# Kernel optimization log

Hardware: AMD Instinct MI355X
Metric: run time of the kernel (lower is better)

## Reference

```python
import jax, jax.numpy as jnp
import numpy as np

D_MODEL = 1024
H = 16
D_K = D_MODEL // H
B = 4
S = 2048


def setup_inputs() -> dict:
    key = jax.random.key(0)
    kq, kk, kv, k1, k2, k3, k4 = jax.random.split(key, 7)
    scale = 1.0 / np.sqrt(D_MODEL)
    inputs = {
        "query": jax.random.normal(kq, (B, S, D_MODEL), dtype=jnp.float32),
        "key": jax.random.normal(kk, (B, S, D_MODEL), dtype=jnp.float32),
        "value": jax.random.normal(kv, (B, S, D_MODEL), dtype=jnp.float32),
        # causal mask: True = masked (upper triangle above diagonal)
        "mask": jnp.triu(jnp.ones((1, 1, S, S), dtype=bool), k=1),
        # nn.Linear weights stored as (out, in); y = x @ W.T
        "w_q": jax.random.normal(k1, (D_MODEL, D_MODEL), dtype=jnp.float32) * scale,
        "w_k": jax.random.normal(k2, (D_MODEL, D_MODEL), dtype=jnp.float32) * scale,
        "w_v": jax.random.normal(k3, (D_MODEL, D_MODEL), dtype=jnp.float32) * scale,
        "w_o": jax.random.normal(k4, (D_MODEL, D_MODEL), dtype=jnp.float32) * scale,
    }
    return inputs


def reference(query, key, value, mask, w_q, w_k, w_v, w_o):
    batch = query.shape[0]

    def split_heads(x):  # (B, S, D) -> (B, H, S, d_k)
        return x.reshape(batch, -1, H, D_K).transpose(0, 2, 1, 3)

    q = split_heads(query @ w_q.T)
    k = split_heads(key @ w_k.T)
    v = split_heads(value @ w_v.T)

    scores = jnp.einsum("bhqd,bhkd->bhqk", q, k) / jnp.sqrt(jnp.float32(D_K))
    scores = jnp.where(mask, -jnp.inf, scores)
    attn = jax.nn.softmax(scores, axis=-1)
    out = jnp.einsum("bhqk,bhkd->bhqd", attn, v)  # (B, H, Sq, d_v)
    out = out.transpose(0, 2, 1, 3).reshape(batch, -1, D_MODEL)
    return out @ w_o.T
```

## Files before the change

### kernel.cpp

```cpp
#include <hip/hip_runtime.h>

typedef unsigned short u16;
typedef __bf16 bf16x8 __attribute__((ext_vector_type(8)));
typedef float f32x4 __attribute__((ext_vector_type(4)));

__device__ __forceinline__ u16 f2bf(float f) {
  union { float f; unsigned u; } v; v.f = f;
  unsigned r = v.u + 0x7fffu + ((v.u >> 16) & 1u);
  return (u16)(r >> 16);
}

__device__ __forceinline__ u16 f2bfn(float f) {
  union { __bf16 h; u16 u; } v; v.h = (__bf16)f; return v.u;
}

__device__ __forceinline__ void gload_lds16(const void* g, void* l) {
  using gvp = const __attribute__((address_space(1))) void*;
  using lvp = __attribute__((address_space(3))) void*;
  __builtin_amdgcn_global_load_lds((gvp)g, (lvp)l, 16, 0, 0);
}

__global__ void cvt_bf16(const float* __restrict__ s0, const float* __restrict__ s1,
                         const float* __restrict__ s2, const float* __restrict__ s3,
                         u16* __restrict__ d0, u16* __restrict__ d1,
                         u16* __restrict__ d2, u16* __restrict__ d3, int n4) {
  const float* srcs[4] = {s0, s1, s2, s3};
  u16* dsts[4] = {d0, d1, d2, d3};
  const float4* src = (const float4*)srcs[blockIdx.y];
  u16* dst = dsts[blockIdx.y];
  for (int i = blockIdx.x * blockDim.x + threadIdx.x; i < n4; i += gridDim.x * blockDim.x) {
    float4 v = src[i];
    ushort4 o;
    o.x = f2bf(v.x); o.y = f2bf(v.y); o.z = f2bf(v.z); o.w = f2bf(v.w);
    *(ushort4*)(dst + (size_t)i * 4) = o;
  }
}

template<int MODE>
__global__ __launch_bounds__(256)
void gemm_bt(const u16* __restrict__ A, const u16* __restrict__ Bw, void* __restrict__ Cout) {
  constexpr int N = 1024, K = 1024, BK = 64;
  __shared__ u16 As[128 * BK];
  __shared__ u16 Bs[128 * BK];
  const int tid = threadIdx.x;
  const int lane = tid & 63, wave = tid >> 6;
  const int wm = wave >> 1, wn = wave & 1;
  const int l15 = lane & 15, lhi = lane >> 4;
  const int m0 = blockIdx.y * 128, n0 = blockIdx.x * 128;
  const int r0 = tid >> 3;
  const int o8 = (tid & 7) * 8;

  f32x4 acc[4][4] = {};

  for (int kt = 0; kt < K / BK; ++kt) {
    const int kb = kt * BK;
#pragma unroll
    for (int c = 0; c < 4; ++c) {
      const int row = c * 32 + r0;
      gload_lds16(A + (m0 + row) * K + kb + o8, (char*)As + (c * 256 + tid) * 16);
      gload_lds16(Bw + (n0 + row) * K + kb + o8, (char*)Bs + (c * 256 + tid) * 16);
    }
    __syncthreads();
#pragma unroll
    for (int kk = 0; kk < 2; ++kk) {
      bf16x8 a[4], b[4];
#pragma unroll
      for (int i = 0; i < 4; ++i)
        a[i] = *(const bf16x8*)(As + (wm * 64 + i * 16 + l15) * BK + kk * 32 + lhi * 8);
#pragma unroll
      for (int j = 0; j < 4; ++j)
        b[j] = *(const bf16x8*)(Bs + (wn * 64 + j * 16 + l15) * BK + kk * 32 + lhi * 8);
#pragma unroll
      for (int i = 0; i < 4; ++i)
#pragma unroll
        for (int j = 0; j < 4; ++j)
          acc[i][j] = __builtin_amdgcn_mfma_f32_16x16x32_bf16(a[i], b[j], acc[i][j], 0, 0, 0);
    }
    __syncthreads();
  }

#pragma unroll
  for (int i = 0; i < 4; ++i) {
#pragma unroll
    for (int j = 0; j < 4; ++j) {
#pragma unroll
      for (int r = 0; r < 4; ++r) {
        const int mg = m0 + wm * 64 + i * 16 + lhi * 4 + r;
        const int ng = n0 + wn * 64 + j * 16 + l15;
        const float v = acc[i][j][r];
        if (MODE == 0) {
          ((float*)Cout)[(size_t)mg * N + ng] = v;
        } else {
          const int b = mg >> 11, s = mg & 2047, h = ng >> 6, dk = ng & 63;
          if (MODE == 1)
            ((u16*)Cout)[(((size_t)(b * 16 + h) * 2048 + s) << 6) + dk] = f2bf(v);
          else
            ((u16*)Cout)[((size_t)(b * 16 + h) * 64 + dk) * 2048 + s] = f2bf(v);
        }
      }
    }
  }
}

__global__ __launch_bounds__(256)
void attn_fwd(const u16* __restrict__ Q, const u16* __restrict__ Kh,
              const u16* __restrict__ Vt, u16* __restrict__ Ao) {
  constexpr int S = 2048;
  constexpr float SCL = 0.125f * 1.44269504088896f;
  __shared__ u16 Ks[2][64 * 64];
  __shared__ u16 Vs[2][64 * 64];
  __shared__ u16 Ps[4][16 * 64];
  const int tid = threadIdx.x;
  const int lane = tid & 63, w = tid >> 6;
  const int l15 = lane & 15, lhi = lane >> 4;
  const int bh = blockIdx.y;
  const int qtA = 31 - (int)blockIdx.x;
  const int qtB = (int)blockIdx.x;

  const u16* QbA = Q + ((size_t)bh * S + qtA * 64 + w * 16 + l15) * 64;
  const u16* QbB = Q + ((size_t)bh * S + qtB * 64 + w * 16 + l15) * 64;
  const bf16x8 qfA0 = *(const bf16x8*)(QbA + lhi * 8);
  const bf16x8 qfA1 = *(const bf16x8*)(QbA + 32 + lhi * 8);
  const bf16x8 qfB0 = *(const bf16x8*)(QbB + lhi * 8);
  const bf16x8 qfB1 = *(const bf16x8*)(QbB + 32 + lhi * 8);

  f32x4 o_acc[4] = {};
  float mrow[4] = {-1e30f, -1e30f, -1e30f, -1e30f};
  float lrow[4] = {0.f, 0.f, 0.f, 0.f};

  const int r0 = tid >> 3;
  const int o16 = (tid & 7) * 16;
  const int gcb = o16 ^ ((r0 & 7) << 4);
  char* PsB = (char*)(Ps[w]);

  auto STAGE = [&](int b, int kt) {
#pragma unroll
    for (int c = 0; c < 2; ++c) {
      const int row = c * 32 + r0;
      gload_lds16((const char*)Kh + ((size_t)(bh * S + kt * 64 + row) * 64) * 2 + gcb,
                  (char*)(Ks[b]) + (c * 256 + tid) * 16);
      gload_lds16((const char*)Vt + ((size_t)(bh * 64 + row) * S + kt * 64) * 2 + gcb,
                  (char*)(Vs[b]) + (c * 256 + tid) * 16);
    }
  };

  const int bb = bh >> 4, hh = bh & 15;
  auto EPILOGUE = [&](int qt) {
#pragma unroll
    for (int r = 0; r < 4; ++r) {
      const float inv = 1.0f / lrow[r];
      const int sg = qt * 64 + w * 16 + lhi * 4 + r;
#pragma unroll
      for (int c = 0; c < 4; ++c)
        Ao[(((size_t)(bb * 2048 + sg) * 16 + hh) << 6) + c * 16 + l15] = f2bfn(o_acc[c][r] * inv);
    }
  };

  const int stepsA = qtA + 1;
  const int total = stepsA + qtB + 1;

  STAGE(0, 0);
  __syncthreads();
  int buf = 0;

  for (int step = 0; step < total; ++step) {
    const bool phB = step >= stepsA;
    const int qt = phB ? qtB : qtA;
    const int kt = phB ? step - stepsA : step;

    if (step + 1 < total)
      STAGE(buf ^ 1, (step + 1 >= stepsA) ? step + 1 - stepsA : step + 1);

    const char* KsB = (const char*)(Ks[buf]);
    const char* VsB = (const char*)(Vs[buf]);
    const bf16x8 q0 = phB ? qfB0 : qfA0;
    const bf16x8 q1 = phB ? qfB1 : qfA1;

    f32x4 sA[4];
    __builtin_amdgcn_s_setprio(1);
#pragma unroll
    for (int c = 0; c < 4; ++c) {
      f32x4 z = {};
      const int krow = c * 16 + l15;
      const int swz = (krow & 7) << 4;
      z = __builtin_amdgcn_mfma_f32_16x16x32_bf16(
          q0, *(const bf16x8*)(KsB + ((krow * 128 + lhi * 16) ^ swz)), z, 0, 0, 0);
      z = __builtin_amdgcn_mfma_f32_16x16x32_bf16(
          q1, *(const bf16x8*)(KsB + ((krow * 128 + 64 + lhi * 16) ^ swz)), z, 0, 0, 0);
      sA[c] = z;
    }
    __builtin_amdgcn_s_setprio(0);

    const bool diag = (kt == qt);
#pragma unroll
    for (int c = 0; c < 4; ++c)
#pragma unroll
      for (int r = 0; r < 4; ++r) {
        float sv = sA[c][r] * SCL;
        if (diag && (c * 16 + l15 > w * 16 + lhi * 4 + r)) sv = -1e30f;
        sA[c][r] = sv;
      }

#pragma unroll
    for (int r = 0; r < 4; ++r) {
      float tm = fmaxf(fmaxf(sA[0][r], sA[1][r]), fmaxf(sA[2][r], sA[3][r]));
      tm = fmaxf(tm, __shfl_xor(tm, 1));
      tm = fmaxf(tm, __shfl_xor(tm, 2));
      tm = fmaxf(tm, __shfl_xor(tm, 4));
      tm = fmaxf(tm, __shfl_xor(tm, 8));
      const float mnew = fmaxf(mrow[r], tm);
      const float sc = __builtin_amdgcn_exp2f(mrow[r] - mnew);
      float rs = 0.f;
#pragma unroll
      for (int c = 0; c < 4; ++c) {
        const float p = __builtin_amdgcn_exp2f(sA[c][r] - mnew);
        sA[c][r] = p;
        rs += p;
      }
      rs += __shfl_xor(rs, 1);
      rs += __shfl_xor(rs, 2);
      rs += __shfl_xor(rs, 4);
      rs += __shfl_xor(rs, 8);
      lrow[r] = lrow[r] * sc + rs;
      mrow[r] = mnew;
#pragma unroll
      for (int c = 0; c < 4; ++c) o_acc[c][r] *= sc;
    }

#pragma unroll
    for (int c = 0; c < 4; ++c)
#pragma unroll
      for (int r = 0; r < 4; ++r) {
        const int prow = lhi * 4 + r;
        *(u16*)(PsB + ((prow * 128 + (c * 16 + l15) * 2) ^ ((prow & 7) << 4))) = f2bfn(sA[c][r]);
      }

    bf16x8 pa0 = *(const bf16x8*)(PsB + ((l15 * 128 + lhi * 16) ^ ((l15 & 7) << 4)));
    bf16x8 pa1 = *(const bf16x8*)(PsB + ((l15 * 128 + 64 + lhi * 16) ^ ((l15 & 7) << 4)));
    __builtin_amdgcn_s_setprio(1);
#pragma unroll
    for (int c = 0; c < 4; ++c) {
      const int drow = c * 16 + l15;
      const int swz = (drow & 7) << 4;
      o_acc[c] = __builtin_amdgcn_mfma_f32_16x16x32_bf16(
          pa0, *(const bf16x8*)(VsB + ((drow * 128 + lhi * 16) ^ swz)), o_acc[c], 0, 0, 0);
      o_acc[c] = __builtin_amdgcn_mfma_f32_16x16x32_bf16(
          pa1, *(const bf16x8*)(VsB + ((drow * 128 + 64 + lhi * 16) ^ swz)), o_acc[c], 0, 0, 0);
    }
    __builtin_amdgcn_s_setprio(0);

    __syncthreads();
    buf ^= 1;

    if (step == stepsA - 1) {
      EPILOGUE(qtA);
#pragma unroll
      for (int r = 0; r < 4; ++r) { mrow[r] = -1e30f; lrow[r] = 0.f; }
#pragma unroll
      for (int c = 0; c < 4; ++c) o_acc[c] = f32x4{};
    }
  }

  EPILOGUE(qtB);
}

extern "C" void kernel_launch(void* const* d_in, const int* in_sizes, int n_in,
                              void* d_out, int out_size, void* d_ws, size_t ws_size,
                              hipStream_t stream) {
  const float* q  = (const float*)d_in[0];
  const float* k  = (const float*)d_in[1];
  const float* v  = (const float*)d_in[2];
  const float* wq = (const float*)d_in[4];
  const float* wk = (const float*)d_in[5];
  const float* wv = (const float*)d_in[6];
  const float* wo = (const float*)d_in[7];

  char* ws = (char*)d_ws;
  const size_t SZX = (size_t)8192 * 1024 * 2;
  const size_t SZW = (size_t)1024 * 1024 * 2;
  u16* Xq = (u16*)(ws);
  u16* Xk = (u16*)(ws + SZX);
  u16* Xv = (u16*)(ws + 2 * SZX);
  u16* Wq = (u16*)(ws + 3 * SZX);
  u16* Wk = (u16*)(ws + 3 * SZX + SZW);
  u16* Wv = (u16*)(ws + 3 * SZX + 2 * SZW);
  u16* Wo = (u16*)(ws + 3 * SZX + 3 * SZW);
  u16* Qh = (u16*)(ws + 3 * SZX + 4 * SZW);
  u16* Kh = (u16*)(ws + 4 * SZX + 4 * SZW);
  u16* Vt = (u16*)(ws + 5 * SZX + 4 * SZW);
  u16* Ao = Xq;

  cvt_bf16<<<dim3(1024, 3), 256, 0, stream>>>(q, k, v, q, Xq, Xk, Xv, Xq, 8388608 / 4);
  cvt_bf16<<<dim3(256, 4), 256, 0, stream>>>(wq, wk, wv, wo, Wq, Wk, Wv, Wo, 1048576 / 4);
  gemm_bt<1><<<dim3(8, 64), 256, 0, stream>>>(Xq, Wq, Qh);
  gemm_bt<1><<<dim3(8, 64), 256, 0, stream>>>(Xk, Wk, Kh);
  gemm_bt<2><<<dim3(8, 64), 256, 0, stream>>>(Xv, Wv, Vt);
  attn_fwd<<<dim3(16, 64), 256, 0, stream>>>(Qh, Kh, Vt, Ao);
  gemm_bt<0><<<dim3(8, 64), 256, 0, stream>>>(Ao, Wo, (float*)d_out);
}
```

Before: 415.3 us.

## Transpose QK^T MFMA so each lane owns one query row for softmax

Swaps the MFMA operands in the QK^T product so the score tile comes out transposed, with each lane holding a single query row spread across its 16 accumulator values. Row max and sum then need mostly in-register reductions plus two cross-lane shuffles instead of four shuffles per row for four rows. P is written to LDS with packed 8-byte stores instead of scalar 2-byte stores. In exchange, the rescale factors must be shuffled back to the output accumulator layout each step and in the epilogue, and the causal mask indexing changes to match.

```diff
diff --git a/kernel.cpp b/kernel.cpp
--- a/kernel.cpp
+++ b/kernel.cpp
@@ -125,8 +125,7 @@
   const bf16x8 qfB1 = *(const bf16x8*)(QbB + 32 + lhi * 8);
 
   f32x4 o_acc[4] = {};
-  float mrow[4] = {-1e30f, -1e30f, -1e30f, -1e30f};
-  float lrow[4] = {0.f, 0.f, 0.f, 0.f};
+  float mrow = -1e30f, lrow = 0.f;
 
   const int r0 = tid >> 3;
   const int o16 = (tid & 7) * 16;
@@ -148,7 +147,7 @@
   auto EPILOGUE = [&](int qt) {
 #pragma unroll
     for (int r = 0; r < 4; ++r) {
-      const float inv = 1.0f / lrow[r];
+      const float inv = 1.0f / __shfl(lrow, lhi * 4 + r);
       const int sg = qt * 64 + w * 16 + lhi * 4 + r;
 #pragma unroll
       for (int c = 0; c < 4; ++c)
@@ -184,9 +183,9 @@
       const int krow = c * 16 + l15;
       const int swz = (krow & 7) << 4;
       z = __builtin_amdgcn_mfma_f32_16x16x32_bf16(
-          q0, *(const bf16x8*)(KsB + ((krow * 128 + lhi * 16) ^ swz)), z, 0, 0, 0);
+          *(const bf16x8*)(KsB + ((krow * 128 + lhi * 16) ^ swz)), q0, z, 0, 0, 0);
       z = __builtin_amdgcn_mfma_f32_16x16x32_bf16(
-          q1, *(const bf16x8*)(KsB + ((krow * 128 + 64 + lhi * 16) ^ swz)), z, 0, 0, 0);
+          *(const bf16x8*)(KsB + ((krow * 128 + 64 + lhi * 16) ^ swz)), q1, z, 0, 0, 0);
       sA[c] = z;
     }
     __builtin_amdgcn_s_setprio(0);
@@ -197,43 +196,53 @@
 #pragma unroll
       for (int r = 0; r < 4; ++r) {
         float sv = sA[c][r] * SCL;
-        if (diag && (c * 16 + l15 > w * 16 + lhi * 4 + r)) sv = -1e30f;
+        if (diag && (c * 16 + lhi * 4 + r > w * 16 + l15)) sv = -1e30f;
         sA[c][r] = sv;
       }
 
-#pragma unroll
-    for (int r = 0; r < 4; ++r) {
-      float tm = fmaxf(fmaxf(sA[0][r], sA[1][r]), fmaxf(sA[2][r], sA[3][r]));
-      tm = fmaxf(tm, __shfl_xor(tm, 1));
-      tm = fmaxf(tm, __shfl_xor(tm, 2));
-      tm = fmaxf(tm, __shfl_xor(tm, 4));
-      tm = fmaxf(tm, __shfl_xor(tm, 8));
-      const float mnew = fmaxf(mrow[r], tm);
-      const float sc = __builtin_amdgcn_exp2f(mrow[r] - mnew);
-      float rs = 0.f;
-#pragma unroll
-      for (int c = 0; c < 4; ++c) {
+    f32x4 m4 = sA[0];
+#pragma unroll
+    for (int c = 1; c < 4; ++c)
+#pragma unroll
+      for (int r = 0; r < 4; ++r) m4[r] = fmaxf(m4[r], sA[c][r]);
+    float tm = fmaxf(fmaxf(m4[0], m4[1]), fmaxf(m4[2], m4[3]));
+    tm = fmaxf(tm, __shfl_xor(tm, 16));
+    tm = fmaxf(tm, __shfl_xor(tm, 32));
+    const float mnew = fmaxf(mrow, tm);
+    const float sc = __builtin_amdgcn_exp2f(mrow - mnew);
+    f32x4 s4 = {};
+#pragma unroll
+    for (int c = 0; c < 4; ++c)
+#pragma unroll
+      for (int r = 0; r < 4; ++r) {
         const float p = __builtin_amdgcn_exp2f(sA[c][r] - mnew);
         sA[c][r] = p;
-        rs += p;
+        s4[r] += p;
       }
-      rs += __shfl_xor(rs, 1);
-      rs += __shfl_xor(rs, 2);
-      rs += __shfl_xor(rs, 4);
-      rs += __shfl_xor(rs, 8);
-      lrow[r] = lrow[r] * sc + rs;
-      mrow[r] = mnew;
-#pragma unroll
-      for (int c = 0; c < 4; ++c) o_acc[c][r] *= sc;
-    }
-
-#pragma unroll
-    for (int c = 0; c < 4; ++c)
-#pragma unroll
-      for (int r = 0; r < 4; ++r) {
-        const int prow = lhi * 4 + r;
-        *(u16*)(PsB + ((prow * 128 + (c * 16 + l15) * 2) ^ ((prow & 7) << 4))) = f2bfn(sA[c][r]);
-      }
+    float rs = (s4[0] + s4[1]) + (s4[2] + s4[3]);
+    rs += __shfl_xor(rs, 16);
+    rs += __shfl_xor(rs, 32);
+    lrow = lrow * sc + rs;
+    mrow = mnew;
+
+    {
+      float scr[4];
+#pragma unroll
+      for (int r = 0; r < 4; ++r) scr[r] = __shfl(sc, lhi * 4 + r);
+#pragma unroll
+      for (int c = 0; c < 4; ++c)
+#pragma unroll
+        for (int r = 0; r < 4; ++r) o_acc[c][r] *= scr[r];
+    }
+
+#pragma unroll
+    for (int c = 0; c < 4; ++c) {
+      union { u16 h[4]; unsigned long long ll; } pk;
+#pragma unroll
+      for (int r = 0; r < 4; ++r) pk.h[r] = f2bfn(sA[c][r]);
+      const int base = l15 * 128 + c * 32 + lhi * 8;
+      *(unsigned long long*)(PsB + (base ^ ((l15 & 7) << 4))) = pk.ll;
+    }
 
     bf16x8 pa0 = *(const bf16x8*)(PsB + ((l15 * 128 + lhi * 16) ^ ((l15 & 7) << 4)));
     bf16x8 pa1 = *(const bf16x8*)(PsB + ((l15 * 128 + 64 + lhi * 16) ^ ((l15 & 7) << 4)));
@@ -254,8 +263,7 @@
 
     if (step == stepsA - 1) {
       EPILOGUE(qtA);
-#pragma unroll
-      for (int r = 0; r < 4; ++r) { mrow[r] = -1e30f; lrow[r] = 0.f; }
+      mrow = -1e30f; lrow = 0.f;
 #pragma unroll
       for (int c = 0; c < 4; ++c) o_acc[c] = f32x4{};
     }
```

After: 360.7 us. 1.15x faster.
